# Optimization experiments

Hardware: AMD Instinct MI355X
Metric: run time of the kernel (lower is better)

Reference implementation:

```python
import jax, jax.numpy as jnp
import numpy as np

D_MODEL = 768
NHEAD = 12
HEAD_DIM = D_MODEL // NHEAD
B, L = 8, 1024


def setup_inputs() -> dict:
    key = jax.random.key(0)
    ks = jax.random.split(key, 10)
    s = 0.02  # init scale for weights
    return {
        "x": jax.random.normal(ks[0], (B, L, D_MODEL), dtype=jnp.float32),
        "pos": jax.random.normal(ks[1], (B, L, D_MODEL), dtype=jnp.float32),
        "qkv_w": jax.random.normal(ks[2], (3 * D_MODEL, D_MODEL), dtype=jnp.float32) * s,
        "qkv_b": jnp.zeros((3 * D_MODEL,), dtype=jnp.float32),
        "pq_w": jax.random.normal(ks[3], (D_MODEL, D_MODEL), dtype=jnp.float32) * s,
        "pq_b": jnp.zeros((D_MODEL,), dtype=jnp.float32),
        "pk_w": jax.random.normal(ks[4], (D_MODEL, D_MODEL), dtype=jnp.float32) * s,
        "pk_b": jnp.zeros((D_MODEL,), dtype=jnp.float32),
    }


def reference(x, pos, qkv_w, qkv_b, pq_w, pq_b, pk_w, pk_b):
    b, l, d = x.shape
    h, hd = NHEAD, HEAD_DIM

    qkv = x @ qkv_w.T + qkv_b  # (b, l, 3d)
    q, k, v = jnp.split(qkv, 3, axis=-1)
    # rearrange 'b l (h d) -> b l h d'
    q = q.reshape(b, l, h, hd)
    k = k.reshape(b, l, h, hd)
    v = v.reshape(b, l, h, hd)

    pq = (pos @ pq_w.T + pq_b).reshape(b, l, h, hd)
    pk = (pos @ pk_w.T + pk_b).reshape(b, l, h, hd)

    CC = jnp.einsum('bnhd,blhd->bhnl', q, k)
    CP = jnp.einsum('bnhd,blhd->bhnl', q, pq)
    PC = jnp.einsum('bnhd,blhd->bhnl', k, pk)

    # Faithful to source: only PC is scaled (operator precedence in original)
    scale = (3 * d) ** 0.5
    attn = jax.nn.softmax(CC + CP + PC / scale, axis=-1)

    out = jnp.einsum('bhnl,blhd->bnhd', attn, v)  # (b, n, h, hd)
    return out
```

## Files before the change

### kernel.cpp

```cpp
#include <hip/hip_runtime.h>

#define NHEAD 12
#define BATCH 8
#define SEQ 1024
#define LOG2E 1.4426950408889634f

typedef __bf16 bf16x8 __attribute__((ext_vector_type(8)));
typedef float  f32x4  __attribute__((ext_vector_type(4)));

#define WAITVM0 asm volatile("s_waitcnt vmcnt(0)" ::: "memory")

__device__ __forceinline__ unsigned short f2bf(float f) {
    union { float f; unsigned u; } v; v.f = f;
    unsigned u = v.u;
    u += 0x7fff + ((u >> 16) & 1);
    return (unsigned short)(u >> 16);
}

__device__ __forceinline__ void gload_lds16(const void* g, void* l) {
    __builtin_amdgcn_global_load_lds(
        (const __attribute__((address_space(1))) unsigned*)g,
        (__attribute__((address_space(3))) unsigned*)l, 16, 0, 0);
}

#define SZ_X    6291456
#define SZ_QKVW 1769472
#define SZ_PW   589824
#define CONV_TOTAL 15532032

__global__ __launch_bounds__(256) void convert_kernel(
    const float* __restrict__ x, const float* __restrict__ pos,
    const float* __restrict__ qkv_w, const float* __restrict__ pq_w,
    const float* __restrict__ pk_w, unsigned short* __restrict__ dst)
{
    const size_t i4 = ((size_t)blockIdx.x * 256 + threadIdx.x) * 4;
    if (i4 >= CONV_TOTAL) return;
    const float* src; size_t off;
    if (i4 < SZ_X)                { src = x;     off = i4; }
    else if (i4 < 2 * SZ_X)       { src = pos;   off = i4 - SZ_X; }
    else if (i4 < 2 * SZ_X + SZ_QKVW) { src = qkv_w; off = i4 - 2 * SZ_X; }
    else if (i4 < 2 * SZ_X + SZ_QKVW + SZ_PW) { src = pq_w; off = i4 - 2 * SZ_X - SZ_QKVW; }
    else                          { src = pk_w;  off = i4 - 2 * SZ_X - SZ_QKVW - SZ_PW; }
    float4 v = *(const float4*)(src + off);
    ushort4 o;
    o.x = f2bf(v.x); o.y = f2bf(v.y); o.z = f2bf(v.z); o.w = f2bf(v.w);
    *(ushort4*)(dst + i4) = o;
}


#define PROJ_STAGE(K0, AS, BS) do {                                          \
    const int k0_ = (K0);                                                    \
    const unsigned short* asrc_; int acol_;                                  \
    if (g == 4)                    { asrc_ = posb; acol_ = k0_; }            \
    else if (g == 3 && k0_ >= 768) { asrc_ = posb; acol_ = k0_ - 768; }      \
    else                           { asrc_ = xb;   acol_ = k0_; }            \
    gload_lds16(asrc_ + (size_t)(m0 + r0) * 768 + acol_ + q0 * 8, &AS[base0]);\
    gload_lds16(asrc_ + (size_t)(m0 + r1) * 768 + acol_ + q1 * 8, &AS[base1]);\
    const unsigned short* wsrc_; int wro_, wco_;                             \
    if (g <= 2)       { wsrc_ = qkvw; wro_ = n0;        wco_ = k0_; }        \
    else if (g == 3) {                                                       \
        if (k0_ < 768) { wsrc_ = qkvw; wro_ = n0 - 1536; wco_ = k0_; }       \
        else           { wsrc_ = pqw;  wro_ = n0 - 2304; wco_ = k0_ - 768; } \
    } else            { wsrc_ = pkw;  wro_ = n0 - 3072; wco_ = k0_; }        \
    gload_lds16(wsrc_ + (size_t)(wro_ + r0) * 768 + wco_ + q0 * 8, &BS[base0]);\
    gload_lds16(wsrc_ + (size_t)(wro_ + r1) * 768 + wco_ + q1 * 8, &BS[base1]);\
} while (0)

#define PROJ_COMPUTE(AS, BS) do {                                            \
    bf16x8 af[4], bfr[4];                                                    \
    _Pragma("unroll")                                                        \
    for (int mt = 0; mt < 4; ++mt) {                                         \
        const int rr = wm + mt * 16 + col16;                                 \
        af[mt] = *(const bf16x8*)&AS[rr * 32 + ((quad ^ ((rr >> 1) & 3)) * 8)];\
    }                                                                        \
    _Pragma("unroll")                                                        \
    for (int nt = 0; nt < 4; ++nt) {                                         \
        const int rr = wn + nt * 16 + col16;                                 \
        bfr[nt] = *(const bf16x8*)&BS[rr * 32 + ((quad ^ ((rr >> 1) & 3)) * 8)];\
    }                                                                        \
    _Pragma("unroll")                                                        \
    for (int mt = 0; mt < 4; ++mt)                                           \
        _Pragma("unroll")                                                    \
        for (int nt = 0; nt < 4; ++nt)                                       \
            acc[mt][nt] = __builtin_amdgcn_mfma_f32_16x16x32_bf16(           \
                af[mt], bfr[nt], acc[mt][nt], 0, 0, 0);                      \
} while (0)

__global__ __launch_bounds__(256) void proj_kernel(
    const unsigned short* __restrict__ xb, const unsigned short* __restrict__ posb,
    const unsigned short* __restrict__ qkvw, const unsigned short* __restrict__ pqw,
    const unsigned short* __restrict__ pkw,
    const float* __restrict__ qkv_b, const float* __restrict__ pq_b,
    const float* __restrict__ pk_b,
    unsigned short* __restrict__ Q2, unsigned short* __restrict__ K2,
    unsigned short* __restrict__ Vt)
{
    __shared__ unsigned short As0[128 * 32];
    __shared__ unsigned short As1[128 * 32];
    __shared__ unsigned short Bs0[128 * 32];
    __shared__ unsigned short Bs1[128 * 32];

    const int m0 = blockIdx.x * 128;
    const int nt30 = ((int)blockIdx.y + 18) % 30;
    const int n0 = nt30 * 128;
    const int g  = n0 / 768;
    const int nk = (g == 3) ? 48 : 24;

    const int tid   = threadIdx.x;
    const int lane  = tid & 63;
    const int w     = tid >> 6;
    const int wm    = (w & 1) * 64;
    const int wn    = (w >> 1) * 64;
    const int quad  = lane >> 4;
    const int col16 = lane & 15;

    const int c0 = w * 64 + lane;
    const int c1 = c0 + 256;
    const int r0 = c0 >> 2, q0 = (c0 & 3) ^ ((c0 >> 3) & 3);
    const int r1 = c1 >> 2, q1 = (c1 & 3) ^ ((c1 >> 3) & 3);
    const int base0 = (w * 64) * 8;
    const int base1 = (w * 64 + 256) * 8;

    f32x4 acc[4][4];
    const f32x4 fzero = {0.f, 0.f, 0.f, 0.f};
#pragma unroll
    for (int mt = 0; mt < 4; ++mt)
#pragma unroll
        for (int nt = 0; nt < 4; ++nt) acc[mt][nt] = fzero;

    PROJ_STAGE(0, As0, Bs0);

    for (int kt = 0; kt < nk; kt += 2) {
        WAITVM0;
        __syncthreads();
        PROJ_STAGE((kt + 1) * 32, As1, Bs1);
        PROJ_COMPUTE(As0, Bs0);

        WAITVM0;
        __syncthreads();
        if (kt + 2 < nk) PROJ_STAGE((kt + 2) * 32, As0, Bs0);
        PROJ_COMPUTE(As1, Bs1);
    }

#pragma unroll
    for (int mt = 0; mt < 4; ++mt) {
        const int mbase = m0 + wm + mt * 16 + quad * 4;
#pragma unroll
        for (int nt = 0; nt < 4; ++nt) {
            const int n = n0 + wn + nt * 16 + col16;
            if (g == 2) {
                const int b = mbase >> 10, l0 = mbase & 1023;
                const int c = n - 1536, h = c >> 6, dd = c & 63;
                ushort4 pk;
                pk.x = f2bf(acc[mt][nt][0] + qkv_b[n]);
                pk.y = f2bf(acc[mt][nt][1] + qkv_b[n]);
                pk.z = f2bf(acc[mt][nt][2] + qkv_b[n]);
                pk.w = f2bf(acc[mt][nt][3] + qkv_b[n]);
                *(ushort4*)&Vt[((size_t)(b * NHEAD + h) * 64 + dd) * 1024 + l0] = pk;
                continue;
            }
#pragma unroll
            for (int r = 0; r < 4; ++r) {
                const int m = mbase + r;
                const int b = m >> 10, l = m & 1023;
                float val = acc[mt][nt][r];
                if (g == 0) {
                    val = (val + qkv_b[n]) * LOG2E;
                    const int h = n >> 6, dd = n & 63;
                    Q2[((size_t)(b * NHEAD + h) * 1024 + l) * 128 + dd] = f2bf(val);
                } else if (g == 1) {
                    val = (val + qkv_b[n]) * (LOG2E / 48.0f);
                    const int c = n - 768, h = c >> 6, dd = c & 63;
                    Q2[((size_t)(b * NHEAD + h) * 1024 + l) * 128 + 64 + dd] = f2bf(val);
                } else if (g == 3) {
                    const int c = n - 2304;
                    val += qkv_b[n - 1536] + pq_b[c];
                    const int h = c >> 6, dd = c & 63;
                    K2[((size_t)(b * NHEAD + h) * 1024 + l) * 128 + dd] = f2bf(val);
                } else {
                    const int c = n - 3072;
                    val += pk_b[c];
                    const int h = c >> 6, dd = c & 63;
                    K2[((size_t)(b * NHEAD + h) * 1024 + l) * 128 + 64 + dd] = f2bf(val);
                }
            }
        }
    }
}


#define ATTN_STAGE(J0, KS, VS) do {                                          \
    const int j0_ = (J0);                                                    \
    gload_lds16(&K2[q2base + (size_t)(j0_ + kr0) * 128 + kc0 * 8], &KS[kbase0]);\
    gload_lds16(&K2[q2base + (size_t)(j0_ + kr1) * 128 + kc1 * 8], &KS[kbase1]);\
    gload_lds16(&Vt[vtbase + (size_t)vr * 1024 + j0_ + vc * 8],    &VS[vbase]);\
} while (0)

#define ATTN_COMPUTE(KS, VS) do {                                            \
    f32x4 st[2][2] = {{fzero, fzero}, {fzero, fzero}};                       \
    _Pragma("unroll")                                                        \
    for (int kk = 0; kk < 4; ++kk) {                                         \
        const int rrj0 = col16, rrj1 = 16 + col16;                           \
        bf16x8 kf0 = *(const bf16x8*)&KS[rrj0 * 128 + (((kk * 4 + quad) ^ (rrj0 & 15)) * 8)];\
        bf16x8 kf1 = *(const bf16x8*)&KS[rrj1 * 128 + (((kk * 4 + quad) ^ (rrj1 & 15)) * 8)];\
        _Pragma("unroll")                                                    \
        for (int qt = 0; qt < 2; ++qt) {                                     \
            st[0][qt] = __builtin_amdgcn_mfma_f32_16x16x32_bf16(kf0, bq[qt][kk], st[0][qt], 0, 0, 0);\
            st[1][qt] = __builtin_amdgcn_mfma_f32_16x16x32_bf16(kf1, bq[qt][kk], st[1][qt], 0, 0, 0);\
        }                                                                    \
    }                                                                        \
    _Pragma("unroll")                                                        \
    for (int qt = 0; qt < 2; ++qt) {                                         \
        float p0[4], p1[4], s = 0.f;                                         \
        _Pragma("unroll")                                                    \
        for (int r = 0; r < 4; ++r) {                                        \
            p0[r] = __builtin_amdgcn_exp2f(st[0][qt][r]);                    \
            p1[r] = __builtin_amdgcn_exp2f(st[1][qt][r]);                    \
            s += p0[r] + p1[r];                                              \
        }                                                                    \
        lsum[qt] += s;                                                       \
        ushort4 pk0, pk1;                                                    \
        pk0.x = f2bf(p0[0]); pk0.y = f2bf(p0[1]); pk0.z = f2bf(p0[2]); pk0.w = f2bf(p0[3]);\
        pk1.x = f2bf(p1[0]); pk1.y = f2bf(p1[1]); pk1.z = f2bf(p1[2]); pk1.w = f2bf(p1[3]);\
        *(ushort4*)&Ps[w][qt * 16 + col16][quad * 4]      = pk0;             \
        *(ushort4*)&Ps[w][qt * 16 + col16][16 + quad * 4] = pk1;             \
    }                                                                        \
    bf16x8 bp[2];                                                            \
    bp[0] = *(const bf16x8*)&Ps[w][col16][quad * 8];                         \
    bp[1] = *(const bf16x8*)&Ps[w][16 + col16][quad * 8];                    \
    _Pragma("unroll")                                                        \
    for (int c2 = 0; c2 < 4; ++c2) {                                         \
        const int rv = c2 * 16 + col16;                                      \
        bf16x8 av = *(const bf16x8*)&VS[rv * 32 + ((quad ^ ((rv >> 2) & 3)) * 8)];\
        _Pragma("unroll")                                                    \
        for (int qt = 0; qt < 2; ++qt)                                       \
            o[qt][c2] = __builtin_amdgcn_mfma_f32_16x16x32_bf16(av, bp[qt], o[qt][c2], 0, 0, 0);\
    }                                                                        \
} while (0)

__global__ __launch_bounds__(256) void attn_kernel(
    const unsigned short* __restrict__ Q2, const unsigned short* __restrict__ K2,
    const unsigned short* __restrict__ Vt, float* __restrict__ out, int b0)
{
    __shared__ unsigned short K2s0[32 * 128];
    __shared__ unsigned short K2s1[32 * 128];
    __shared__ unsigned short Vts0[64 * 32];
    __shared__ unsigned short Vts1[64 * 32];
    __shared__ unsigned short Ps[4][32][40];

    const int bh_l = blockIdx.x;
    const int b = b0 + bh_l / NHEAD, h = bh_l % NHEAD;
    const int tid   = threadIdx.x;
    const int lane  = tid & 63;
    const int w     = tid >> 6;
    const int quad  = lane >> 4;
    const int col16 = lane & 15;
    const int qbase = blockIdx.y * 128 + w * 32;

    const size_t q2base = (size_t)bh_l * 1024 * 128;
    const size_t vtbase = (size_t)bh_l * 64 * 1024;

    const int kL0 = w * 64 + lane, kL1 = kL0 + 256;
    const int kr0 = kL0 >> 4, kc0 = (kL0 & 15) ^ (kr0 & 15);
    const int kr1 = kL1 >> 4, kc1 = (kL1 & 15) ^ (kr1 & 15);
    const int vL  = w * 64 + lane;
    const int vr  = vL >> 2,  vc  = (vL & 3) ^ ((vL >> 4) & 3);
    const int kbase0 = (w * 64) * 8, kbase1 = (w * 64 + 256) * 8;
    const int vbase  = (w * 64) * 8;

    bf16x8 bq[2][4];
#pragma unroll
    for (int qt = 0; qt < 2; ++qt)
#pragma unroll
        for (int kk = 0; kk < 4; ++kk)
            bq[qt][kk] = *(const bf16x8*)&Q2[q2base +
                (size_t)(qbase + qt * 16 + col16) * 128 + kk * 32 + quad * 8];

    f32x4 o[2][4];
    const f32x4 fzero = {0.f, 0.f, 0.f, 0.f};
#pragma unroll
    for (int qt = 0; qt < 2; ++qt)
#pragma unroll
        for (int c2 = 0; c2 < 4; ++c2) o[qt][c2] = fzero;
    float lsum[2] = {0.f, 0.f};

    ATTN_STAGE(0, K2s0, Vts0);

    for (int it = 0; it < SEQ / 32; it += 2) {
        WAITVM0;
        __syncthreads();
        ATTN_STAGE((it + 1) * 32, K2s1, Vts1);
        ATTN_COMPUTE(K2s0, Vts0);

        WAITVM0;
        __syncthreads();
        if (it + 2 < SEQ / 32) ATTN_STAGE((it + 2) * 32, K2s0, Vts0);
        ATTN_COMPUTE(K2s1, Vts1);
    }

#pragma unroll
    for (int qt = 0; qt < 2; ++qt) {
        lsum[qt] += __shfl_xor(lsum[qt], 16, 64);
        lsum[qt] += __shfl_xor(lsum[qt], 32, 64);
    }

#pragma unroll
    for (int qt = 0; qt < 2; ++qt) {
        const float inv = 1.0f / lsum[qt];
        const int q = qbase + qt * 16 + col16;
#pragma unroll
        for (int c2 = 0; c2 < 4; ++c2) {
#pragma unroll
            for (int r = 0; r < 4; ++r) {
                const int dd = c2 * 16 + quad * 4 + r;
                out[(((size_t)(b * 1024 + q)) * 12 + h) * 64 + dd] = o[qt][c2][r] * inv;
            }
        }
    }
}

extern "C" void kernel_launch(void* const* d_in, const int* in_sizes, int n_in,
                              void* d_out, int out_size, void* d_ws, size_t ws_size,
                              hipStream_t stream) {
    const float* x     = (const float*)d_in[0];
    const float* pos   = (const float*)d_in[1];
    const float* qkv_w = (const float*)d_in[2];
    const float* qkv_b = (const float*)d_in[3];
    const float* pq_w  = (const float*)d_in[4];
    const float* pq_b  = (const float*)d_in[5];
    const float* pk_w  = (const float*)d_in[6];
    const float* pk_b  = (const float*)d_in[7];
    float* out = (float*)d_out;

    unsigned short* ws   = (unsigned short*)d_ws;
    unsigned short* xb   = ws;
    unsigned short* posb = xb + SZ_X;
    unsigned short* qkvw = posb + SZ_X;
    unsigned short* pqw  = qkvw + SZ_QKVW;
    unsigned short* pkw  = pqw + SZ_PW;
    unsigned short* cbuf = pkw + SZ_PW;

    const size_t conv_bytes = (size_t)CONV_TOTAL * 2;
    const size_t per_batch  = (size_t)NHEAD * 1024 * 128 * 4
                            + (size_t)NHEAD * 64 * 1024 * 2;
    int cb = BATCH;
    while (cb > 1 && conv_bytes + (size_t)cb * per_batch > ws_size) cb >>= 1;

    unsigned short* Q2 = cbuf;
    unsigned short* K2 = Q2 + (size_t)cb * NHEAD * 1024 * 128;
    unsigned short* Vt = K2 + (size_t)cb * NHEAD * 1024 * 128;

    convert_kernel<<<(CONV_TOTAL / 4 + 255) / 256, 256, 0, stream>>>(
        x, pos, qkv_w, pq_w, pk_w, ws);

    for (int b0 = 0; b0 < BATCH; b0 += cb) {
        proj_kernel<<<dim3(cb * 8, 30), 256, 0, stream>>>(
            xb + (size_t)b0 * 1024 * 768, posb + (size_t)b0 * 1024 * 768,
            qkvw, pqw, pkw, qkv_b, pq_b, pk_b, Q2, K2, Vt);
        attn_kernel<<<dim3(cb * NHEAD, 8), 256, 0, stream>>>(Q2, K2, Vt, out, b0);
    }
}
```

Measured before the change: 272.2 us.

## Deepen global-to-LDS pipelines to four stages with partial vmcnt waits

Both the projection GEMM and attention kernels go from double-buffered LDS staging with full vmcnt(0) waits to a four-buffer ring. Three tiles are prefetched ahead and partial vmcnt waits let later loads stay in flight. The aim is to hide global-load latency behind MFMA compute. In exchange, LDS use roughly doubles, which may reduce occupancy, and the hardcoded vmcnt counts must match the number of loads each stage issues.

```diff
diff --git a/kernel.cpp b/kernel.cpp
--- a/kernel.cpp
+++ b/kernel.cpp
@@ -8,7 +8,7 @@
 typedef __bf16 bf16x8 __attribute__((ext_vector_type(8)));
 typedef float  f32x4  __attribute__((ext_vector_type(4)));
 
-#define WAITVM0 asm volatile("s_waitcnt vmcnt(0)" ::: "memory")
+#define VMWAIT(N) asm volatile("s_waitcnt vmcnt(" #N ")" ::: "memory")
 
 __device__ __forceinline__ unsigned short f2bf(float f) {
     union { float f; unsigned u; } v; v.f = f;
@@ -97,8 +97,12 @@
 {
     __shared__ unsigned short As0[128 * 32];
     __shared__ unsigned short As1[128 * 32];
+    __shared__ unsigned short As2[128 * 32];
+    __shared__ unsigned short As3[128 * 32];
     __shared__ unsigned short Bs0[128 * 32];
     __shared__ unsigned short Bs1[128 * 32];
+    __shared__ unsigned short Bs2[128 * 32];
+    __shared__ unsigned short Bs3[128 * 32];
 
     const int m0 = blockIdx.x * 128;
     const int nt30 = ((int)blockIdx.y + 18) % 30;
@@ -128,19 +132,25 @@
 #pragma unroll
         for (int nt = 0; nt < 4; ++nt) acc[mt][nt] = fzero;
 
-    PROJ_STAGE(0, As0, Bs0);
-
-    for (int kt = 0; kt < nk; kt += 2) {
-        WAITVM0;
-        __syncthreads();
-        PROJ_STAGE((kt + 1) * 32, As1, Bs1);
-        PROJ_COMPUTE(As0, Bs0);
-
-        WAITVM0;
-        __syncthreads();
-        if (kt + 2 < nk) PROJ_STAGE((kt + 2) * 32, As0, Bs0);
-        PROJ_COMPUTE(As1, Bs1);
-    }
+    PROJ_STAGE(0,  As0, Bs0);
+    PROJ_STAGE(32, As1, Bs1);
+    PROJ_STAGE(64, As2, Bs2);
+
+    for (int s = 0; s < nk - 4; s += 4) {
+        VMWAIT(8); __syncthreads();
+        PROJ_STAGE((s + 3) * 32, As3, Bs3); PROJ_COMPUTE(As0, Bs0);
+        VMWAIT(8); __syncthreads();
+        PROJ_STAGE((s + 4) * 32, As0, Bs0); PROJ_COMPUTE(As1, Bs1);
+        VMWAIT(8); __syncthreads();
+        PROJ_STAGE((s + 5) * 32, As1, Bs1); PROJ_COMPUTE(As2, Bs2);
+        VMWAIT(8); __syncthreads();
+        PROJ_STAGE((s + 6) * 32, As2, Bs2); PROJ_COMPUTE(As3, Bs3);
+    }
+    VMWAIT(8); __syncthreads();
+    PROJ_STAGE((nk - 1) * 32, As3, Bs3); PROJ_COMPUTE(As0, Bs0);
+    VMWAIT(8); __syncthreads(); PROJ_COMPUTE(As1, Bs1);
+    VMWAIT(4); __syncthreads(); PROJ_COMPUTE(As2, Bs2);
+    VMWAIT(0); __syncthreads(); PROJ_COMPUTE(As3, Bs3);
 
 #pragma unroll
     for (int mt = 0; mt < 4; ++mt) {
@@ -242,10 +252,14 @@
     const unsigned short* __restrict__ Q2, const unsigned short* __restrict__ K2,
     const unsigned short* __restrict__ Vt, float* __restrict__ out, int b0)
 {
-    __shared__ unsigned short K2s0[32 * 128];
-    __shared__ unsigned short K2s1[32 * 128];
-    __shared__ unsigned short Vts0[64 * 32];
-    __shared__ unsigned short Vts1[64 * 32];
+    __shared__ unsigned short K2sA[32 * 128];
+    __shared__ unsigned short K2sB[32 * 128];
+    __shared__ unsigned short K2sC[32 * 128];
+    __shared__ unsigned short K2sD[32 * 128];
+    __shared__ unsigned short VtsA[64 * 32];
+    __shared__ unsigned short VtsB[64 * 32];
+    __shared__ unsigned short VtsC[64 * 32];
+    __shared__ unsigned short VtsD[64 * 32];
     __shared__ unsigned short Ps[4][32][40];
 
     const int bh_l = blockIdx.x;
@@ -284,19 +298,25 @@
         for (int c2 = 0; c2 < 4; ++c2) o[qt][c2] = fzero;
     float lsum[2] = {0.f, 0.f};
 
-    ATTN_STAGE(0, K2s0, Vts0);
-
-    for (int it = 0; it < SEQ / 32; it += 2) {
-        WAITVM0;
-        __syncthreads();
-        ATTN_STAGE((it + 1) * 32, K2s1, Vts1);
-        ATTN_COMPUTE(K2s0, Vts0);
-
-        WAITVM0;
-        __syncthreads();
-        if (it + 2 < SEQ / 32) ATTN_STAGE((it + 2) * 32, K2s0, Vts0);
-        ATTN_COMPUTE(K2s1, Vts1);
-    }
+    ATTN_STAGE(0,  K2sA, VtsA);
+    ATTN_STAGE(32, K2sB, VtsB);
+    ATTN_STAGE(64, K2sC, VtsC);
+
+    for (int s = 0; s < SEQ / 32 - 4; s += 4) {
+        VMWAIT(6); __syncthreads();
+        ATTN_STAGE((s + 3) * 32, K2sD, VtsD); ATTN_COMPUTE(K2sA, VtsA);
+        VMWAIT(6); __syncthreads();
+        ATTN_STAGE((s + 4) * 32, K2sA, VtsA); ATTN_COMPUTE(K2sB, VtsB);
+        VMWAIT(6); __syncthreads();
+        ATTN_STAGE((s + 5) * 32, K2sB, VtsB); ATTN_COMPUTE(K2sC, VtsC);
+        VMWAIT(6); __syncthreads();
+        ATTN_STAGE((s + 6) * 32, K2sC, VtsC); ATTN_COMPUTE(K2sD, VtsD);
+    }
+    VMWAIT(6); __syncthreads();
+    ATTN_STAGE(SEQ - 32, K2sD, VtsD); ATTN_COMPUTE(K2sA, VtsA);
+    VMWAIT(6); __syncthreads(); ATTN_COMPUTE(K2sB, VtsB);
+    VMWAIT(3); __syncthreads(); ATTN_COMPUTE(K2sC, VtsC);
+    VMWAIT(0); __syncthreads(); ATTN_COMPUTE(K2sD, VtsD);
 
 #pragma unroll
     for (int qt = 0; qt < 2; ++qt) {
```

Result: slower. 290.5 us (+6.7%).
